# Kernel optimization log

Measured on AMD Instinct MI355X. Metric: run time of the kernel, lower is better.

The kernel has to match this reference:

```python
import jax, jax.numpy as jnp
import numpy as np

RANK = 16
ALPHA = 16.0
SCALING = ALPHA / RANK
N_ADAPTERS = 8
IN_F = 4096
OUT_F = 4096
BATCH = 4
SEQ = 2048


def setup_inputs() -> dict:
    key = jax.random.key(0)
    kx, ka, kb, ki = jax.random.split(key, 4)
    x = jax.random.normal(kx, (BATCH, SEQ, IN_F), dtype=jnp.float32)
    # A init: randn * 0.02 (as in module). B is zeros in the module; use small
    # random values here so the baseline output/grads are non-trivial.
    A = jax.random.normal(ka, (N_ADAPTERS, OUT_F, RANK), dtype=jnp.float32) * 0.02
    B = jax.random.normal(kb, (N_ADAPTERS, RANK, IN_F), dtype=jnp.float32) * 0.02
    adapter_ids = jax.random.randint(ki, (BATCH,), 0, N_ADAPTERS, dtype=jnp.int32)
    return {"x": x, "A": A, "B": B, "adapter_ids": adapter_ids}


def reference(x, A, B, adapter_ids):
    # Original: Bx = einsum('bni,ari->bnar', x, B); res = einsum('bnar,aor->bnao', Bx, A)
    # then res[arange(b), :, adapter_ids] * scaling.
    # Equivalent (gather-then-batched-GEMM): select each batch element's adapter
    # first, avoiding the O(n_adapters) dense intermediate. Same math.
    B_sel = B[adapter_ids]            # [b, r, in]
    A_sel = A[adapter_ids]            # [b, out, r]
    Bx = jnp.einsum('bni,bri->bnr', x, B_sel)   # [b, n, r]
    out = jnp.einsum('bnr,bor->bno', Bx, A_sel)  # [b, n, out]
    return out * SCALING
```

## Files before the change

### kernel.cpp

```cpp
#include <hip/hip_runtime.h>
#include <hip/hip_bf16.h>

#define RANK   16
#define IN_F   4096
#define OUT_F  4096
#define NROWS  8192

typedef __bf16 bf16x8  __attribute__((ext_vector_type(8)));
typedef float  floatx4 __attribute__((ext_vector_type(4)));

__device__ float g_bx[NROWS * RANK];

static __device__ __forceinline__ bf16x8 cvt8(floatx4 a, floatx4 b) {
    bf16x8 r;
    r[0] = (__bf16)a[0]; r[1] = (__bf16)a[1]; r[2] = (__bf16)a[2]; r[3] = (__bf16)a[3];
    r[4] = (__bf16)b[0]; r[5] = (__bf16)b[1]; r[6] = (__bf16)b[2]; r[7] = (__bf16)b[3];
    return r;
}

__global__ __launch_bounds__(512, 4) void
lora_bx_kernel(const float* __restrict__ x, const float* __restrict__ Bw,
               const int* __restrict__ ids)
{
    const int tile = blockIdx.x;
    const int row0 = tile * 16;
    const int adapter = ids[row0 >> 11];
    const int tid  = threadIdx.x;
    const int wave = tid >> 6;
    const int lane = tid & 63;

    __shared__ float red[8][256];

    const int m    = lane & 15;
    const int quad = lane >> 4;
    const int k0   = wave * 512 + quad * 8;
    const float* xp = x + (size_t)(row0 + m) * IN_F + k0;
    const float* bp = Bw + (size_t)adapter * (RANK * IN_F) + m * IN_F + k0;

    floatx4 acc = {0.f, 0.f, 0.f, 0.f};
#pragma unroll
    for (int s = 0; s < 16; ++s) {
        floatx4 xa = *reinterpret_cast<const floatx4*>(xp + s * 32);
        floatx4 xb = *reinterpret_cast<const floatx4*>(xp + s * 32 + 4);
        floatx4 ba = *reinterpret_cast<const floatx4*>(bp + s * 32);
        floatx4 bb = *reinterpret_cast<const floatx4*>(bp + s * 32 + 4);
        acc = __builtin_amdgcn_mfma_f32_16x16x32_bf16(
            cvt8(xa, xb), cvt8(ba, bb), acc, 0, 0, 0);
    }
#pragma unroll
    for (int j = 0; j < 4; ++j)
        red[wave][(quad * 4 + j) * 16 + m] = acc[j];
    __syncthreads();
    if (tid < 256) {
        float s = ((red[0][tid] + red[1][tid]) + (red[2][tid] + red[3][tid]))
                + ((red[4][tid] + red[5][tid]) + (red[6][tid] + red[7][tid]));
        g_bx[tile * 256 + tid] = s;
    }
}

__global__ __launch_bounds__(256, 4) void
lora_out_kernel(const float* __restrict__ Aw, const int* __restrict__ ids,
                float* __restrict__ out)
{
    const int b    = blockIdx.x;
    const int cc   = b & 3;
    const int rg   = b >> 2;
    const int row0 = rg * 32;
    const int adapter = ids[row0 >> 11];
    const int tid  = threadIdx.x;
    const int wave = tid >> 6;
    const int lane = tid & 63;
    const int c0   = cc * 1024 + wave * 256 + lane * 4;

    const float* ap = Aw + ((size_t)adapter * OUT_F + c0) * RANK;
    floatx4 a[16];
#pragma unroll
    for (int i = 0; i < 16; ++i)
        a[i] = *reinterpret_cast<const floatx4*>(ap + i * 4);

#pragma unroll 2
    for (int rr = 0; rr < 32; ++rr) {
        const int row = row0 + rr;
        const float* bp = g_bx + (size_t)row * RANK;
        const floatx4 b0 = *reinterpret_cast<const floatx4*>(bp);
        const floatx4 b1 = *reinterpret_cast<const floatx4*>(bp + 4);
        const floatx4 b2 = *reinterpret_cast<const floatx4*>(bp + 8);
        const floatx4 b3 = *reinterpret_cast<const floatx4*>(bp + 12);
        floatx4 ov;
#pragma unroll
        for (int j = 0; j < 4; ++j) {
            const floatx4 a0 = a[j * 4 + 0], a1 = a[j * 4 + 1];
            const floatx4 a2 = a[j * 4 + 2], a3 = a[j * 4 + 3];
            float s = a0[0] * b0[0] + a0[1] * b0[1] + a0[2] * b0[2] + a0[3] * b0[3]
                    + a1[0] * b1[0] + a1[1] * b1[1] + a1[2] * b1[2] + a1[3] * b1[3]
                    + a2[0] * b2[0] + a2[1] * b2[1] + a2[2] * b2[2] + a2[3] * b2[3]
                    + a3[0] * b3[0] + a3[1] * b3[1] + a3[2] * b3[2] + a3[3] * b3[3];
            ov[j] = s;
        }
        __builtin_nontemporal_store(
            ov, reinterpret_cast<floatx4*>(out + (size_t)row * OUT_F + c0));
    }
}

extern "C" void kernel_launch(void* const* d_in, const int* in_sizes, int n_in,
                              void* d_out, int out_size, void* d_ws, size_t ws_size,
                              hipStream_t stream) {
    const float* x   = (const float*)d_in[0];
    const float* Aw  = (const float*)d_in[1];
    const float* Bw  = (const float*)d_in[2];
    const int*   ids = (const int*)d_in[3];
    float* out = (float*)d_out;

    lora_bx_kernel <<<dim3(NROWS / 16), dim3(512), 0, stream>>>(x, Bw, ids);
    lora_out_kernel<<<dim3(1024),       dim3(256), 0, stream>>>(Aw, ids, out);
}
```

Before: 251.9 us.

## Stage x tiles into LDS via async global_load_lds with double buffering

The Bx kernel now streams x through double-buffered shared memory using async global-to-LDS loads in 512-column chunks. A swizzled LDS layout is used to avoid bank conflicts, and all waves cover the whole K range in contiguous chunks instead of each wave owning a strided K slice. The goal is fully coalesced row-contiguous loads of x and overlap of memory with MFMA compute. The cost is a block barrier per chunk and a much larger LDS footprint, which may lower occupancy.

```diff
diff --git a/kernel.cpp b/kernel.cpp
--- a/kernel.cpp
+++ b/kernel.cpp
@@ -5,6 +5,8 @@
 #define IN_F   4096
 #define OUT_F  4096
 #define NROWS  8192
+#define CHUNK  512
+#define NCH    (IN_F / CHUNK)
 
 typedef __bf16 bf16x8  __attribute__((ext_vector_type(8)));
 typedef float  floatx4 __attribute__((ext_vector_type(4)));
@@ -18,6 +20,12 @@
     return r;
 }
 
+static __device__ __forceinline__ void stage16(const float* g, float* l) {
+    __builtin_amdgcn_global_load_lds(
+        (const __attribute__((address_space(1))) void*)g,
+        (__attribute__((address_space(3))) void*)l, 16, 0, 0);
+}
+
 __global__ __launch_bounds__(512, 4) void
 lora_bx_kernel(const float* __restrict__ x, const float* __restrict__ Bw,
                const int* __restrict__ ids)
@@ -28,25 +36,58 @@
     const int tid  = threadIdx.x;
     const int wave = tid >> 6;
     const int lane = tid & 63;
+    const int m    = lane & 15;
+    const int quad = lane >> 4;
 
+    __shared__ float xs[2][16][CHUNK];
     __shared__ float red[8][256];
 
-    const int m    = lane & 15;
-    const int quad = lane >> 4;
-    const int k0   = wave * 512 + quad * 8;
-    const float* xp = x + (size_t)(row0 + m) * IN_F + k0;
-    const float* bp = Bw + (size_t)adapter * (RANK * IN_F) + m * IN_F + k0;
+    const int r0 = 2 * wave, r1 = r0 + 1;
+    const int so0 = (((lane * 16) ^ ((r0 & 7) << 4)) >> 2);
+    const int so1 = (((lane * 16) ^ ((r1 & 7) << 4)) >> 2);
+    const float* xrow0 = x + (size_t)(row0 + r0) * IN_F;
+    const float* xrow1 = x + (size_t)(row0 + r1) * IN_F;
 
+    auto STAGE = [&](int c, int bf) {
+        const float* s0 = xrow0 + c * CHUNK;
+        const float* s1 = xrow1 + c * CHUNK;
+        stage16(s0 +       so0, &xs[bf][r0][0]);
+        stage16(s0 + 256 + so0, &xs[bf][r0][256]);
+        stage16(s1 +       so1, &xs[bf][r1][0]);
+        stage16(s1 + 256 + so1, &xs[bf][r1][256]);
+    };
+
+    const float* bp = Bw + (size_t)adapter * (RANK * IN_F) + m * IN_F
+                    + wave * 64 + quad * 8;
+    const int Cm = (m & 7) << 4;
     floatx4 acc = {0.f, 0.f, 0.f, 0.f};
+
+    STAGE(0, 0);
+    for (int c = 0; c < NCH; ++c) {
+        const int bf = c & 1;
+        const float* bc = bp + c * CHUNK;
+        floatx4 B00 = *reinterpret_cast<const floatx4*>(bc);
+        floatx4 B01 = *reinterpret_cast<const floatx4*>(bc + 4);
+        floatx4 B10 = *reinterpret_cast<const floatx4*>(bc + 32);
+        floatx4 B11 = *reinterpret_cast<const floatx4*>(bc + 36);
+        const bf16x8 bb0 = cvt8(B00, B01);
+        const bf16x8 bb1 = cvt8(B10, B11);
+
+        __syncthreads();
+        if (c + 1 < NCH) STAGE(c + 1, bf ^ 1);
+
+        const char* base = (const char*)xs + (size_t)bf * (16 * CHUNK * 4);
+        const char* rowb = base + m * (CHUNK * 4);
 #pragma unroll
-    for (int s = 0; s < 16; ++s) {
-        floatx4 xa = *reinterpret_cast<const floatx4*>(xp + s * 32);
-        floatx4 xb = *reinterpret_cast<const floatx4*>(xp + s * 32 + 4);
-        floatx4 ba = *reinterpret_cast<const floatx4*>(bp + s * 32);
-        floatx4 bb = *reinterpret_cast<const floatx4*>(bp + s * 32 + 4);
-        acc = __builtin_amdgcn_mfma_f32_16x16x32_bf16(
-            cvt8(xa, xb), cvt8(ba, bb), acc, 0, 0, 0);
+        for (int s = 0; s < 2; ++s) {
+            const int ka = wave * 256 + s * 128 + quad * 32;
+            floatx4 xa = *reinterpret_cast<const floatx4*>(rowb + ((ka     ) ^ Cm));
+            floatx4 xb = *reinterpret_cast<const floatx4*>(rowb + ((ka + 16) ^ Cm));
+            acc = __builtin_amdgcn_mfma_f32_16x16x32_bf16(
+                cvt8(xa, xb), (s == 0) ? bb0 : bb1, acc, 0, 0, 0);
+        }
     }
+
 #pragma unroll
     for (int j = 0; j < 4; ++j)
         red[wave][(quad * 4 + j) * 16 + m] = acc[j];
```

New measurement: 248.9 us. About the same (-1.2%).

## Fuse LoRA kernels into one pipelined kernel overlapping Bx compute with output writes

Applied to the files above, without the earlier changes.

Merges the Bx reduction kernel and the output-expansion kernel into one kernel, so each block handles two 16-row tiles. The second tile's Bx MFMA loop is interleaved with writing the first tile's output rows, and intermediates stay in shared memory rather than a global buffer. This removes a kernel launch boundary and the global round trip for Bx, and overlaps the x reads with the output writes. The cost is only 256 blocks for the whole device, which may leave many CUs idle, plus heavier register pressure and a serial tail for the second tile's output.

```diff
diff --git a/kernel.cpp b/kernel.cpp
--- a/kernel.cpp
+++ b/kernel.cpp
@@ -5,11 +5,10 @@
 #define IN_F   4096
 #define OUT_F  4096
 #define NROWS  8192
+#define NBLK   256
 
 typedef __bf16 bf16x8  __attribute__((ext_vector_type(8)));
 typedef float  floatx4 __attribute__((ext_vector_type(4)));
-
-__device__ float g_bx[NROWS * RANK];
 
 static __device__ __forceinline__ bf16x8 cvt8(floatx4 a, floatx4 b) {
     bf16x8 r;
@@ -18,88 +17,109 @@
     return r;
 }
 
-__global__ __launch_bounds__(512, 4) void
-lora_bx_kernel(const float* __restrict__ x, const float* __restrict__ Bw,
-               const int* __restrict__ ids)
+__global__ __launch_bounds__(512, 2) void
+lora_pipe_kernel(const float* __restrict__ x, const float* __restrict__ Aw,
+                 const float* __restrict__ Bw, const int* __restrict__ ids,
+                 float* __restrict__ out)
 {
-    const int tile = blockIdx.x;
-    const int row0 = tile * 16;
-    const int adapter = ids[row0 >> 11];
+    const int blk  = blockIdx.x;
+    const int row0 = (blk * 2)     * 16;
+    const int row1 = (blk * 2 + 1) * 16;
+    const int ad0  = ids[row0 >> 11];
+    const int ad1  = ids[row1 >> 11];
     const int tid  = threadIdx.x;
     const int wave = tid >> 6;
     const int lane = tid & 63;
+    const int m    = lane & 15;
+    const int quad = lane >> 4;
 
     __shared__ float red[8][256];
+    __shared__ float bxs[2][256];
 
-    const int m    = lane & 15;
-    const int quad = lane >> 4;
-    const int k0   = wave * 512 + quad * 8;
-    const float* xp = x + (size_t)(row0 + m) * IN_F + k0;
-    const float* bp = Bw + (size_t)adapter * (RANK * IN_F) + m * IN_F + k0;
+    const int koff = wave * 512 + quad * 8;
+    const float* xp0 = x + (size_t)(row0 + m) * IN_F + koff;
+    const float* xp1 = x + (size_t)(row1 + m) * IN_F + koff;
+    const float* bp0 = Bw + (size_t)ad0 * (RANK * IN_F) + m * IN_F + koff;
+    const float* bp1 = Bw + (size_t)ad1 * (RANK * IN_F) + m * IN_F + koff;
 
-    floatx4 acc = {0.f, 0.f, 0.f, 0.f};
-#pragma unroll
-    for (int s = 0; s < 16; ++s) {
-        floatx4 xa = *reinterpret_cast<const floatx4*>(xp + s * 32);
-        floatx4 xb = *reinterpret_cast<const floatx4*>(xp + s * 32 + 4);
-        floatx4 ba = *reinterpret_cast<const floatx4*>(bp + s * 32);
-        floatx4 bb = *reinterpret_cast<const floatx4*>(bp + s * 32 + 4);
-        acc = __builtin_amdgcn_mfma_f32_16x16x32_bf16(
-            cvt8(xa, xb), cvt8(ba, bb), acc, 0, 0, 0);
-    }
-#pragma unroll
-    for (int j = 0; j < 4; ++j)
-        red[wave][(quad * 4 + j) * 16 + m] = acc[j];
-    __syncthreads();
-    if (tid < 256) {
-        float s = ((red[0][tid] + red[1][tid]) + (red[2][tid] + red[3][tid]))
-                + ((red[4][tid] + red[5][tid]) + (red[6][tid] + red[7][tid]));
-        g_bx[tile * 256 + tid] = s;
-    }
-}
+    const int cbase = wave * 256 + lane * 4;
 
-__global__ __launch_bounds__(256, 4) void
-lora_out_kernel(const float* __restrict__ Aw, const int* __restrict__ ids,
-                float* __restrict__ out)
-{
-    const int b    = blockIdx.x;
-    const int cc   = b & 3;
-    const int rg   = b >> 2;
-    const int row0 = rg * 32;
-    const int adapter = ids[row0 >> 11];
-    const int tid  = threadIdx.x;
-    const int wave = tid >> 6;
-    const int lane = tid & 63;
-    const int c0   = cc * 1024 + wave * 256 + lane * 4;
-
-    const float* ap = Aw + ((size_t)adapter * OUT_F + c0) * RANK;
     floatx4 a[16];
-#pragma unroll
-    for (int i = 0; i < 16; ++i)
-        a[i] = *reinterpret_cast<const floatx4*>(ap + i * 4);
-
-#pragma unroll 2
-    for (int rr = 0; rr < 32; ++rr) {
-        const int row = row0 + rr;
-        const float* bp = g_bx + (size_t)row * RANK;
-        const floatx4 b0 = *reinterpret_cast<const floatx4*>(bp);
-        const floatx4 b1 = *reinterpret_cast<const floatx4*>(bp + 4);
-        const floatx4 b2 = *reinterpret_cast<const floatx4*>(bp + 8);
-        const floatx4 b3 = *reinterpret_cast<const floatx4*>(bp + 12);
+    auto p2row = [&](int buf, int rowb, int c0, int rr) {
+        const float* bx = &bxs[buf][rr * 16];
+        const floatx4 b0 = *reinterpret_cast<const floatx4*>(bx);
+        const floatx4 b1 = *reinterpret_cast<const floatx4*>(bx + 4);
+        const floatx4 b2 = *reinterpret_cast<const floatx4*>(bx + 8);
+        const floatx4 b3 = *reinterpret_cast<const floatx4*>(bx + 12);
         floatx4 ov;
 #pragma unroll
         for (int j = 0; j < 4; ++j) {
             const floatx4 a0 = a[j * 4 + 0], a1 = a[j * 4 + 1];
             const floatx4 a2 = a[j * 4 + 2], a3 = a[j * 4 + 3];
-            float s = a0[0] * b0[0] + a0[1] * b0[1] + a0[2] * b0[2] + a0[3] * b0[3]
-                    + a1[0] * b1[0] + a1[1] * b1[1] + a1[2] * b1[2] + a1[3] * b1[3]
-                    + a2[0] * b2[0] + a2[1] * b2[1] + a2[2] * b2[2] + a2[3] * b2[3]
-                    + a3[0] * b3[0] + a3[1] * b3[1] + a3[2] * b3[2] + a3[3] * b3[3];
-            ov[j] = s;
+            ov[j] = a0[0]*b0[0] + a0[1]*b0[1] + a0[2]*b0[2] + a0[3]*b0[3]
+                  + a1[0]*b1[0] + a1[1]*b1[1] + a1[2]*b1[2] + a1[3]*b1[3]
+                  + a2[0]*b2[0] + a2[1]*b2[1] + a2[2]*b2[2] + a2[3]*b2[3]
+                  + a3[0]*b3[0] + a3[1]*b3[1] + a3[2]*b3[2] + a3[3]*b3[3];
         }
         __builtin_nontemporal_store(
-            ov, reinterpret_cast<floatx4*>(out + (size_t)row * OUT_F + c0));
+            ov, reinterpret_cast<floatx4*>(out + (size_t)(rowb + rr) * OUT_F + c0));
+    };
+    auto loadA = [&](int ad, int c0) {
+        const float* ap = Aw + ((size_t)ad * OUT_F + c0) * RANK;
+#pragma unroll
+        for (int i = 0; i < 16; ++i)
+            a[i] = *reinterpret_cast<const floatx4*>(ap + i * 4);
+    };
+    auto reduceTo = [&](int buf, floatx4 acc) {
+#pragma unroll
+        for (int j = 0; j < 4; ++j)
+            red[wave][(quad * 4 + j) * 16 + m] = acc[j];
+        __syncthreads();
+        if (tid < 256) {
+            float s = ((red[0][tid] + red[1][tid]) + (red[2][tid] + red[3][tid]))
+                    + ((red[4][tid] + red[5][tid]) + (red[6][tid] + red[7][tid]));
+            bxs[buf][tid] = s;
+        }
+        __syncthreads();
+    };
+
+    floatx4 acc = {0.f, 0.f, 0.f, 0.f};
+#pragma unroll
+    for (int s = 0; s < 16; ++s) {
+        floatx4 xa = *reinterpret_cast<const floatx4*>(xp0 + s * 32);
+        floatx4 xb = *reinterpret_cast<const floatx4*>(xp0 + s * 32 + 4);
+        floatx4 ba = *reinterpret_cast<const floatx4*>(bp0 + s * 32);
+        floatx4 bb = *reinterpret_cast<const floatx4*>(bp0 + s * 32 + 4);
+        acc = __builtin_amdgcn_mfma_f32_16x16x32_bf16(
+            cvt8(xa, xb), cvt8(ba, bb), acc, 0, 0, 0);
     }
+    reduceTo(0, acc);
+
+    loadA(ad0, cbase);
+    acc = (floatx4){0.f, 0.f, 0.f, 0.f};
+#pragma unroll
+    for (int s = 0; s < 16; ++s) {
+        floatx4 xa = *reinterpret_cast<const floatx4*>(xp1 + s * 32);
+        floatx4 xb = *reinterpret_cast<const floatx4*>(xp1 + s * 32 + 4);
+        floatx4 ba = *reinterpret_cast<const floatx4*>(bp1 + s * 32);
+        floatx4 bb = *reinterpret_cast<const floatx4*>(bp1 + s * 32 + 4);
+        if (s == 8) loadA(ad0, 2048 + cbase);
+        const int pass = s >> 3;
+        const int c0   = pass * 2048 + cbase;
+        const int rr   = (2 * s) & 15;
+        p2row(0, row0, c0, rr);
+        p2row(0, row0, c0, rr + 1);
+        acc = __builtin_amdgcn_mfma_f32_16x16x32_bf16(
+            cvt8(xa, xb), cvt8(ba, bb), acc, 0, 0, 0);
+    }
+    reduceTo(1, acc);
+
+    loadA(ad1, cbase);
+#pragma unroll 4
+    for (int rr = 0; rr < 16; ++rr) p2row(1, row1, cbase, rr);
+    loadA(ad1, 2048 + cbase);
+#pragma unroll 4
+    for (int rr = 0; rr < 16; ++rr) p2row(1, row1, 2048 + cbase, rr);
 }
 
 extern "C" void kernel_launch(void* const* d_in, const int* in_sizes, int n_in,
@@ -111,6 +131,5 @@
     const int*   ids = (const int*)d_in[3];
     float* out = (float*)d_out;
 
-    lora_bx_kernel <<<dim3(NROWS / 16), dim3(512), 0, stream>>>(x, Bw, ids);
-    lora_out_kernel<<<dim3(1024),       dim3(256), 0, stream>>>(Aw, ids, out);
+    lora_pipe_kernel<<<dim3(NBLK), dim3(512), 0, stream>>>(x, Aw, Bw, ids, out);
 }
```

Measured after the change: 256.8 us. Within noise of the previous version (+2.0%).
